# Kernel tuning notes

Measured on AMD Instinct MI355X. Metric: run time of the kernel, lower is better.

## Reference

```python
import math
import jax, jax.numpy as jnp
import numpy as np

EMBED = 1024
HEADS = 16
DEPTH = 12
HEAD_DIM = EMBED // HEADS // 2  # 32
LAMBDA_INIT = 0.8 - 0.6 * math.exp(-0.3 * DEPTH)


def setup_inputs() -> dict:
    key = jax.random.key(0)
    ks = jax.random.split(key, 11)
    B, T, S = 2, 2048, 2048
    std = 1.0 / math.sqrt(EMBED)
    return {
        "query_x": jax.random.normal(ks[0], (B, T, EMBED), jnp.float32),
        "kv_x": jax.random.normal(ks[1], (B, S, EMBED), jnp.float32),
        "Wq": jax.random.normal(ks[2], (EMBED, EMBED), jnp.float32) * std,
        "Wk": jax.random.normal(ks[3], (EMBED, EMBED), jnp.float32) * std,
        "Wv": jax.random.normal(ks[4], (EMBED, EMBED), jnp.float32) * std,
        "Wo": jax.random.normal(ks[5], (EMBED, EMBED), jnp.float32) * std,
        "lambda_q1": jax.random.normal(ks[6], (HEAD_DIM,), jnp.float32) * 0.1,
        "lambda_k1": jax.random.normal(ks[7], (HEAD_DIM,), jnp.float32) * 0.1,
        "lambda_q2": jax.random.normal(ks[8], (HEAD_DIM,), jnp.float32) * 0.1,
        "lambda_k2": jax.random.normal(ks[9], (HEAD_DIM,), jnp.float32) * 0.1,
        "subln_w": jnp.ones((2 * HEAD_DIM,), jnp.float32),
    }


def rms_norm(x, w, eps=1e-5):
    xf = x.astype(jnp.float32)
    out = xf * jax.lax.rsqrt(jnp.mean(xf * xf, axis=-1, keepdims=True) + eps)
    return out.astype(x.dtype) * w


def reference(query_x, kv_x, Wq, Wk, Wv, Wo, lambda_q1, lambda_k1, lambda_q2, lambda_k2, subln_w):
    B, T, _ = query_x.shape
    S = kv_x.shape[1]
    H, D = HEADS, HEAD_DIM
    scaling = D ** -0.5

    q = (query_x @ Wq).reshape(B, T, 2 * H, D).transpose(0, 2, 1, 3)  # [B,2H,T,D]
    k = (kv_x @ Wk).reshape(B, S, 2 * H, D).transpose(0, 2, 1, 3)     # [B,2H,S,D]
    v = (kv_x @ Wv).reshape(B, S, H, 2 * D).transpose(0, 2, 1, 3)     # [B,H,S,2D]

    scores = jnp.einsum("bhtd,bhsd->bhts", q * scaling, k)            # [B,2H,T,S]
    attn_w = jax.nn.softmax(scores.astype(jnp.float32), axis=-1).astype(scores.dtype)

    lambda_1 = jnp.exp(jnp.sum(lambda_q1 * lambda_k1).astype(jnp.float32))
    lambda_2 = jnp.exp(jnp.sum(lambda_q2 * lambda_k2).astype(jnp.float32))
    lambda_full = (lambda_1 - lambda_2 + LAMBDA_INIT).astype(q.dtype)

    attn_w = attn_w.reshape(B, H, 2, T, S)
    attn_w = attn_w[:, :, 0] - lambda_full * attn_w[:, :, 1]          # [B,H,T,S]

    attn = jnp.einsum("bhts,bhse->bhte", attn_w, v)                   # [B,H,T,2D]
    attn = rms_norm(attn, subln_w) * (1.0 - LAMBDA_INIT)
    attn = attn.transpose(0, 2, 1, 3).reshape(B, T, H * 2 * D)
    return attn @ Wo
```

## Files before the change

### kernel.cpp

```cpp
#include <hip/hip_runtime.h>
#include <stdint.h>


#define LAMBDA_INIT_F 0.7836057665316245f
#define OUT_SCALE_F   0.2163942334683755f
#define QK_SCALE_F    0.17677669529663687f
#define LOG2E_F       1.4426950408889634f

typedef _Float16 f16x8 __attribute__((ext_vector_type(8)));
typedef _Float16 f16x4 __attribute__((ext_vector_type(4)));
typedef _Float16 f16x2 __attribute__((ext_vector_type(2)));
typedef __fp16   h16x2 __attribute__((ext_vector_type(2)));
typedef float    f32x4 __attribute__((ext_vector_type(4)));
typedef float    f32x16 __attribute__((ext_vector_type(16)));

__device__ inline void gl_lds16(const void* g, void* l) {
  __builtin_amdgcn_global_load_lds(
      (const __attribute__((address_space(1))) void*)g,
      (__attribute__((address_space(3))) void*)l, 16, 0, 0);
}

__device__ inline f16x2 cvtpk(float a, float b) {
  h16x2 r = __builtin_amdgcn_cvt_pkrtz(a, b);
  return __builtin_bit_cast(f16x2, r);
}

__global__ __launch_bounds__(256) void prep(
    const float* __restrict__ qx, const float* __restrict__ kvx,
    const float* __restrict__ Wq, const float* __restrict__ Wk,
    const float* __restrict__ Wv, const float* __restrict__ Wo,
    const float* __restrict__ lq1, const float* __restrict__ lk1,
    const float* __restrict__ lq2, const float* __restrict__ lk2,
    _Float16* __restrict__ xq, _Float16* __restrict__ xkv,
    _Float16* __restrict__ WqT, _Float16* __restrict__ WkT,
    _Float16* __restrict__ WvT, _Float16* __restrict__ WoT,
    float* __restrict__ lamv) {
  __shared__ _Float16 t[64][65];
  const int bb = blockIdx.x;
  const int tid = threadIdx.x;
  if (bb < 8192) {
    const float* src = (bb < 4096) ? qx : kvx;
    _Float16* dst = (bb < 4096) ? xq : xkv;
    int i = ((bb & 4095) * 256 + tid) * 4;
    float4 v = *(const float4*)(src + i);
    f16x4 o;
    o[0] = (_Float16)v.x; o[1] = (_Float16)v.y;
    o[2] = (_Float16)v.z; o[3] = (_Float16)v.w;
    *(f16x4*)(dst + i) = o;
  } else if (bb < 9216) {
    const int idx = bb - 8192;
    const int w = idx >> 8, loc = idx & 255;
    const float* W = (w == 0) ? Wq : (w == 1) ? Wk : (w == 2) ? Wv : Wo;
    _Float16* Wt   = (w == 0) ? WqT : (w == 1) ? WkT : (w == 2) ? WvT : WoT;
    const float scale = (w == 0) ? QK_SCALE_F * LOG2E_F : 1.0f;
    const int nb = (loc & 15) * 64, kb2 = (loc >> 4) * 64;
#pragma unroll
    for (int p = 0; p < 16; ++p) {
      int i = p * 256 + tid;
      int r = i >> 6, c = i & 63;
      t[c][r] = (_Float16)(W[(size_t)(kb2 + r) * 1024 + nb + c] * scale);
    }
    __syncthreads();
#pragma unroll
    for (int p = 0; p < 16; ++p) {
      int i = p * 256 + tid;
      int r = i >> 6, c = i & 63;
      Wt[(size_t)(nb + r) * 1024 + kb2 + c] = t[r][c];
    }
  } else {
    if (tid < 64) {
      int l = tid;
      float a = (l < 32) ? lq1[l] * lk1[l] : 0.f;
      float b = (l < 32) ? lq2[l] * lk2[l] : 0.f;
#pragma unroll
      for (int m = 1; m < 64; m <<= 1) {
        a += __shfl_xor(a, m, 64);
        b += __shfl_xor(b, m, 64);
      }
      if (l == 0) lamv[0] = expf(a) - expf(b) + LAMBDA_INIT_F;
    }
  }
}

__global__ __launch_bounds__(256, 4) void gemmseg(
    const _Float16* __restrict__ A0, const _Float16* __restrict__ B0, _Float16* __restrict__ C0,
    const _Float16* __restrict__ A1, const _Float16* __restrict__ B1, _Float16* __restrict__ C1,
    const _Float16* __restrict__ A2, const _Float16* __restrict__ B2, _Float16* __restrict__ C2,
    int nseg, float* __restrict__ Cf32) {
  __shared__ alignas(16) _Float16 As[2][4096];
  __shared__ alignas(16) _Float16 Bs[2][4096];
  const int tid = threadIdx.x;
  const int lane = tid & 63, wid = tid >> 6;
  const int g = lane >> 4, ln = lane & 15;
  const int wm = wid >> 1, wn = wid & 1;

  const int nwg = nseg << 8;
  const int b0 = blockIdx.x;
  const int swz = (b0 & 7) * (nwg >> 3) + (b0 >> 3);
  const int seg = swz >> 8, loc = swz & 255;
  const _Float16 *A, *B;
  _Float16* C;
  if (seg == 0)      { A = A0; B = B0; C = C0; }
  else if (seg == 1) { A = A1; B = B1; C = C1; }
  else               { A = A2; B = B2; C = C2; }
  int bm, bn, N;
  if (seg == 2) { N = 4096; bm = (loc >> 5) << 7; bn = (loc & 31) << 7; }
  else          { N = 1024; bm = (loc >> 3) << 7; bn = (loc & 7) << 7; }
  const int K = 1024;

  f32x4 acc[4][4];
#pragma unroll
  for (int i = 0; i < 4; ++i)
#pragma unroll
    for (int j = 0; j < 4; ++j) acc[i][j] = (f32x4){0.f, 0.f, 0.f, 0.f};

  int aoff[4], boff[4];
#pragma unroll
  for (int i = 0; i < 4; ++i) {
    int r = wm * 64 + i * 16 + ln;
    aoff[i] = r * 32 + (((g + ((r >> 1) & 3)) & 3) << 3);
    r = wn * 64 + i * 16 + ln;
    boff[i] = r * 32 + (((g + ((r >> 1) & 3)) & 3) << 3);
  }

  auto STAGE = [&](int buf, int kt) {
#pragma unroll
    for (int l2 = 0; l2 < 2; ++l2) {
      int ci = l2 * 256 + wid * 64 + lane;
      int r = ci >> 2, cp = ci & 3;
      int c = (cp - ((r >> 1) & 3)) & 3;
      gl_lds16(A + (size_t)(bm + r) * K + kt + c * 8,
               (void*)&As[buf][l2 * 2048 + wid * 512]);
      gl_lds16(B + (size_t)(bn + r) * K + kt + c * 8,
               (void*)&Bs[buf][l2 * 2048 + wid * 512]);
    }
  };

  STAGE(0, 0);
  __syncthreads();
  int buf = 0;
  for (int kt = 0; kt < K; kt += 32) {
    if (kt + 32 < K) STAGE(buf ^ 1, kt + 32);
    f16x8 af[4], bf[4];
#pragma unroll
    for (int i = 0; i < 4; ++i) {
      af[i] = *(const f16x8*)(&As[buf][aoff[i]]);
      bf[i] = *(const f16x8*)(&Bs[buf][boff[i]]);
    }
#pragma unroll
    for (int i = 0; i < 4; ++i)
#pragma unroll
      for (int j = 0; j < 4; ++j)
        acc[i][j] = __builtin_amdgcn_mfma_f32_16x16x32_f16(af[i], bf[j], acc[i][j], 0, 0, 0);
    __syncthreads();
    buf ^= 1;
  }

#pragma unroll
  for (int i = 0; i < 4; ++i) {
#pragma unroll
    for (int j = 0; j < 4; ++j) {
      int grow = bm + wm * 64 + i * 16 + g * 4;
      int gcol = bn + wn * 64 + j * 16 + ln;
#pragma unroll
      for (int r = 0; r < 4; ++r) {
        if (Cf32) Cf32[(size_t)(grow + r) * N + gcol] = acc[i][j][r];
        else      C[(size_t)(grow + r) * N + gcol] = (_Float16)acc[i][j][r];
      }
    }
  }
}

__global__ __launch_bounds__(512, 4) void diffattn(const _Float16* __restrict__ qb,
                                                   const _Float16* __restrict__ kb,
                                                   const _Float16* __restrict__ vT,
                                                   const float* __restrict__ lam_p,
                                                   const float* __restrict__ subw,
                                                   _Float16* __restrict__ attn16) {
  __shared__ alignas(16) _Float16 stg[2][8192];

  const int tid = threadIdx.x;
  const int lane = tid & 63, wid = tid >> 6;
  const int q32 = lane & 31;
  const int hl = lane >> 5;
  const int wq = wid & 1;
  const int comp = (wid >> 1) & 1;
  const int sh = wid >> 2;
  const int bid = blockIdx.x;
  const int wg = ((bid & 7) << 7) | (bid >> 3);
  const int qt = wg & 31;
  const int h = (wg >> 5) & 15;
  const int b = wg >> 9;
  const int trow = qt * 64 + wq * 32 + q32;

  const _Float16* qp = qb + ((size_t)b * 2048 + trow) * 1024 + (2 * h + comp) * 32 + hl * 8;
  f16x8 qf_0 = *(const f16x8*)(qp);
  f16x8 qf_1 = *(const f16x8*)(qp + 16);

  const _Float16* kg;
  {
    const int r = (wid & 1) * 16 + (lane >> 2);
    const int pos = lane & 3;
    const int c = (pos - ((r >> 1) & 3)) & 3;
    kg = kb + ((size_t)b * 2048 + (size_t)(wid >> 2) * 1024 + r) * 1024 +
         (2 * h + ((wid >> 1) & 1)) * 32 + c * 8;
  }
  const _Float16* vg;
  {
    const int e = wid * 8 + (lane >> 3);
    const int pos = lane & 7;
    const int ca = (pos - (e & 7)) & 7;
    vg = vT + ((size_t)(h * 64 + e)) * 4096 + (size_t)b * 2048 +
         (ca >> 2) * 1024 + (ca & 3) * 8;
  }

  const int kreg = (sh * 2 + comp) * 1024;
  const int sk = (q32 >> 1) & 3;
  const int ko0 = kreg + q32 * 32 + ((hl + sk) & 3) * 8;
  const int ko1 = kreg + q32 * 32 + ((2 + hl + sk) & 3) * 8;
  const int e7 = q32 & 7;
  const int vb0 = 4096 + q32 * 64 + hl * 4;
  const int vp0 = ((sh * 4 + 0 + e7) & 7) * 8;
  const int vp1 = ((sh * 4 + 1 + e7) & 7) * 8;
  const int vp2 = ((sh * 4 + 2 + e7) & 7) * 8;
  const int vp3 = ((sh * 4 + 3 + e7) & 7) * 8;

  f32x16 O[2] = {};
  float m = 0.f, l = 0.f;
  const f32x16 zf = {};

  auto STAGE = [&](int buf, int it) {
    gl_lds16(kg + (size_t)it * 32768, (void*)&stg[buf][wid * 512]);
    gl_lds16(vg + it * 32,            (void*)&stg[buf][4096 + wid * 512]);
  };

  auto PROC = [&](int buf) {
    const _Float16* sb = &stg[buf][0];
    f16x8 Kf0 = *(const f16x8*)(sb + ko0);
    f16x8 Kf1 = *(const f16x8*)(sb + ko1);

    __builtin_amdgcn_s_setprio(1);
    f32x16 st = __builtin_amdgcn_mfma_f32_32x32x16_f16(Kf0, qf_0, zf, 0, 0, 0);
    st = __builtin_amdgcn_mfma_f32_32x32x16_f16(Kf1, qf_1, st, 0, 0, 0);
    __builtin_amdgcn_s_setprio(0);

    float p[16];
#pragma unroll
    for (int i = 0; i < 16; ++i) p[i] = __builtin_amdgcn_exp2f(st[i]);
    float s8[8];
#pragma unroll
    for (int i = 0; i < 8; ++i) s8[i] = p[2 * i] + p[2 * i + 1];
#pragma unroll
    for (int i = 0; i < 4; ++i) s8[i] += s8[i + 4];
    float rs = (s8[0] + s8[1]) + (s8[2] + s8[3]);
    l += rs + __shfl_xor(rs, 32, 64);

    union { f16x8 v; f16x2 h2[4]; } pb0, pb1;
    pb0.h2[0] = cvtpk(p[0], p[1]);   pb0.h2[1] = cvtpk(p[2], p[3]);
    pb0.h2[2] = cvtpk(p[4], p[5]);   pb0.h2[3] = cvtpk(p[6], p[7]);
    pb1.h2[0] = cvtpk(p[8], p[9]);   pb1.h2[1] = cvtpk(p[10], p[11]);
    pb1.h2[2] = cvtpk(p[12], p[13]); pb1.h2[3] = cvtpk(p[14], p[15]);

    const _Float16* v0 = sb + vb0;
    const _Float16* v1 = sb + vb0 + 2048;
    union { f16x8 v; f16x4 h4[2]; } va00, va01, va10, va11;
    va00.h4[0] = *(const f16x4*)(v0 + vp0); va00.h4[1] = *(const f16x4*)(v0 + vp1);
    va01.h4[0] = *(const f16x4*)(v1 + vp0); va01.h4[1] = *(const f16x4*)(v1 + vp1);
    va10.h4[0] = *(const f16x4*)(v0 + vp2); va10.h4[1] = *(const f16x4*)(v0 + vp3);
    va11.h4[0] = *(const f16x4*)(v1 + vp2); va11.h4[1] = *(const f16x4*)(v1 + vp3);

    __builtin_amdgcn_s_setprio(1);
    O[0] = __builtin_amdgcn_mfma_f32_32x32x16_f16(va00.v, pb0.v, O[0], 0, 0, 0);
    O[1] = __builtin_amdgcn_mfma_f32_32x32x16_f16(va01.v, pb0.v, O[1], 0, 0, 0);
    O[0] = __builtin_amdgcn_mfma_f32_32x32x16_f16(va10.v, pb1.v, O[0], 0, 0, 0);
    O[1] = __builtin_amdgcn_mfma_f32_32x32x16_f16(va11.v, pb1.v, O[1], 0, 0, 0);
    __builtin_amdgcn_s_setprio(0);
  };

  STAGE(0, 0);
  __syncthreads();
  int buf = 0;
  for (int it = 0; it < 32; ++it) {
    if (it + 1 < 32) STAGE(buf ^ 1, it + 1);
    PROC(buf);
    __syncthreads();
    buf ^= 1;
  }

  float* pay = (float*)&stg[0][0];
  _Float16* o2s = (_Float16*)(pay + 2 * 64 * 34);

  if (comp == 1 && sh == 1) {
    float* d = pay + (wq * 64 + lane) * 34;
#pragma unroll
    for (int t2 = 0; t2 < 2; ++t2)
#pragma unroll
      for (int i = 0; i < 16; ++i) d[t2 * 16 + i] = O[t2][i];
    d[32] = m; d[33] = l;
  }
  __syncthreads();
  if (comp == 1 && sh == 0) {
    const float* d = pay + (wq * 64 + lane) * 34;
    float mb = d[32], lb = d[33];
    float mn = fmaxf(m, mb);
    float ca = __builtin_amdgcn_exp2f(m - mn);
    float cb = __builtin_amdgcn_exp2f(mb - mn);
    m = mn; l = l * ca + lb * cb;
#pragma unroll
    for (int t2 = 0; t2 < 2; ++t2)
#pragma unroll
      for (int i = 0; i < 16; ++i) O[t2][i] = O[t2][i] * ca + d[t2 * 16 + i] * cb;
  }
  __syncthreads();
  if (comp == 0 && sh == 1) {
    float* d = pay + (wq * 64 + lane) * 34;
#pragma unroll
    for (int t2 = 0; t2 < 2; ++t2)
#pragma unroll
      for (int i = 0; i < 16; ++i) d[t2 * 16 + i] = O[t2][i];
    d[32] = m; d[33] = l;
  }
  if (comp == 1 && sh == 0) {
    float rl = 1.f / l;
    _Float16* d = o2s + (wq * 64 + lane) * 32;
#pragma unroll
    for (int t2 = 0; t2 < 2; ++t2)
#pragma unroll
      for (int i = 0; i < 16; ++i) d[t2 * 16 + i] = (_Float16)(O[t2][i] * rl);
  }
  __syncthreads();
  if (comp != 0 || sh != 0) return;

  {
    const float* d = pay + (wq * 64 + lane) * 34;
    float mb = d[32], lb = d[33];
    float mn = fmaxf(m, mb);
    float ca = __builtin_amdgcn_exp2f(m - mn);
    float cb = __builtin_amdgcn_exp2f(mb - mn);
    l = l * ca + lb * cb;
#pragma unroll
    for (int t2 = 0; t2 < 2; ++t2)
#pragma unroll
      for (int i = 0; i < 16; ++i) O[t2][i] = O[t2][i] * ca + d[t2 * 16 + i] * cb;
  }

  const float lam = lam_p[0];
  const _Float16* d2 = o2s + (wq * 64 + lane) * 32;
  float rl = 1.f / l;
  float x[2][16];
  float ssq = 0.f;
#pragma unroll
  for (int et = 0; et < 2; ++et)
#pragma unroll
    for (int i = 0; i < 16; ++i) {
      float v = O[et][i] * rl - lam * (float)d2[et * 16 + i];
      x[et][i] = v;
      ssq += v * v;
    }
  ssq += __shfl_xor(ssq, 32, 64);
  float rms = rsqrtf(ssq * (1.f / 64.f) + 1e-5f) * OUT_SCALE_F;

  _Float16* orow = attn16 + ((size_t)b * 2048 + trow) * 1024 + h * 64;
#pragma unroll
  for (int et = 0; et < 2; ++et)
#pragma unroll
    for (int grp = 0; grp < 4; ++grp) {
      int e0 = et * 32 + grp * 8 + 4 * hl;
      float4 w = *(const float4*)(subw + e0);
      f16x4 o;
      o[0] = (_Float16)(x[et][grp * 4 + 0] * rms * w.x);
      o[1] = (_Float16)(x[et][grp * 4 + 1] * rms * w.y);
      o[2] = (_Float16)(x[et][grp * 4 + 2] * rms * w.z);
      o[3] = (_Float16)(x[et][grp * 4 + 3] * rms * w.w);
      *(f16x4*)(orow + e0) = o;
    }
}

extern "C" void kernel_launch(void* const* d_in, const int* in_sizes, int n_in,
                              void* d_out, int out_size, void* d_ws, size_t ws_size,
                              hipStream_t stream) {
  const float* query_x = (const float*)d_in[0];
  const float* kv_x    = (const float*)d_in[1];
  const float* Wq      = (const float*)d_in[2];
  const float* Wk      = (const float*)d_in[3];
  const float* Wv      = (const float*)d_in[4];
  const float* Wo      = (const float*)d_in[5];
  const float* lq1     = (const float*)d_in[6];
  const float* lk1     = (const float*)d_in[7];
  const float* lq2     = (const float*)d_in[8];
  const float* lk2     = (const float*)d_in[9];
  const float* subw    = (const float*)d_in[10];
  float* out = (float*)d_out;

  const size_t NX = (size_t)4096 * 1024;
  const size_t NW = (size_t)1024 * 1024;
  _Float16* xq  = (_Float16*)d_ws;
  _Float16* xkv = xq  + NX;
  _Float16* WqT = xkv + NX;
  _Float16* WkT = WqT + NW;
  _Float16* WvT = WkT + NW;
  _Float16* WoT = WvT + NW;
  _Float16* qb  = WoT + NW;
  _Float16* kbf = qb  + NX;
  _Float16* vTb = kbf + NX;
  _Float16* a16 = vTb + NX;
  float* lamv   = (float*)(a16 + NX);

  prep<<<9217, 256, 0, stream>>>(query_x, kv_x, Wq, Wk, Wv, Wo,
                                 lq1, lk1, lq2, lk2,
                                 xq, xkv, WqT, WkT, WvT, WoT, lamv);

  gemmseg<<<768, 256, 0, stream>>>(xq, WqT, qb,
                                   xkv, WkT, kbf,
                                   WvT, xkv, vTb,
                                   3, nullptr);

  diffattn<<<1024, 512, 0, stream>>>(qb, kbf, vTb, lamv, subw, a16);

  gemmseg<<<256, 256, 0, stream>>>(a16, WoT, nullptr,
                                   nullptr, nullptr, nullptr,
                                   nullptr, nullptr, nullptr,
                                   1, out);
}
```

Baseline: 156.0 us.

## Process two query sub-tiles per attention block to reuse staged K/V tiles

Each attention workgroup now covers 128 query rows instead of 64. Every wave holds two Q fragments and issues twice the MFMAs against each staged K/V tile, which halves the grid and the global-to-LDS K/V traffic per query row. The combine epilogue drops the unused running-max rescaling and becomes plain sums, then runs twice, once per sub-tile. In exchange the kernel needs more registers (launch bounds lowered to 2 blocks per SM) and has fewer blocks in flight, which may reduce latency hiding.

```diff
diff --git a/kernel.cpp b/kernel.cpp
--- a/kernel.cpp
+++ b/kernel.cpp
@@ -171,7 +171,7 @@
   }
 }
 
-__global__ __launch_bounds__(512, 4) void diffattn(const _Float16* __restrict__ qb,
+__global__ __launch_bounds__(512, 2) void diffattn(const _Float16* __restrict__ qb,
                                                    const _Float16* __restrict__ kb,
                                                    const _Float16* __restrict__ vT,
                                                    const float* __restrict__ lam_p,
@@ -187,15 +187,18 @@
   const int comp = (wid >> 1) & 1;
   const int sh = wid >> 2;
   const int bid = blockIdx.x;
-  const int wg = ((bid & 7) << 7) | (bid >> 3);
-  const int qt = wg & 31;
-  const int h = (wg >> 5) & 15;
-  const int b = wg >> 9;
-  const int trow = qt * 64 + wq * 32 + q32;
-
-  const _Float16* qp = qb + ((size_t)b * 2048 + trow) * 1024 + (2 * h + comp) * 32 + hl * 8;
-  f16x8 qf_0 = *(const f16x8*)(qp);
-  f16x8 qf_1 = *(const f16x8*)(qp + 16);
+  const int wg = ((bid & 7) << 6) | (bid >> 3);
+  const int qt = wg & 15;
+  const int h = (wg >> 4) & 15;
+  const int b = wg >> 8;
+  const int trowA = qt * 128 + wq * 64 + q32;
+
+  const _Float16* qpA = qb + ((size_t)b * 2048 + trowA) * 1024 + (2 * h + comp) * 32 + hl * 8;
+  f16x8 qfA0 = *(const f16x8*)(qpA);
+  f16x8 qfA1 = *(const f16x8*)(qpA + 16);
+  const _Float16* qpB = qpA + (size_t)32 * 1024;
+  f16x8 qfB0 = *(const f16x8*)(qpB);
+  f16x8 qfB1 = *(const f16x8*)(qpB + 16);
 
   const _Float16* kg;
   {
@@ -225,8 +228,8 @@
   const int vp2 = ((sh * 4 + 2 + e7) & 7) * 8;
   const int vp3 = ((sh * 4 + 3 + e7) & 7) * 8;
 
-  f32x16 O[2] = {};
-  float m = 0.f, l = 0.f;
+  f32x16 OA[2] = {}, OB[2] = {};
+  float lpA = 0.f, lpB = 0.f;
   const f32x16 zf = {};
 
   auto STAGE = [&](int buf, int it) {
@@ -240,40 +243,64 @@
     f16x8 Kf1 = *(const f16x8*)(sb + ko1);
 
     __builtin_amdgcn_s_setprio(1);
-    f32x16 st = __builtin_amdgcn_mfma_f32_32x32x16_f16(Kf0, qf_0, zf, 0, 0, 0);
-    st = __builtin_amdgcn_mfma_f32_32x32x16_f16(Kf1, qf_1, st, 0, 0, 0);
+    f32x16 stA = __builtin_amdgcn_mfma_f32_32x32x16_f16(Kf0, qfA0, zf, 0, 0, 0);
+    stA = __builtin_amdgcn_mfma_f32_32x32x16_f16(Kf1, qfA1, stA, 0, 0, 0);
+    f32x16 stB = __builtin_amdgcn_mfma_f32_32x32x16_f16(Kf0, qfB0, zf, 0, 0, 0);
+    stB = __builtin_amdgcn_mfma_f32_32x32x16_f16(Kf1, qfB1, stB, 0, 0, 0);
     __builtin_amdgcn_s_setprio(0);
 
-    float p[16];
-#pragma unroll
-    for (int i = 0; i < 16; ++i) p[i] = __builtin_amdgcn_exp2f(st[i]);
-    float s8[8];
-#pragma unroll
-    for (int i = 0; i < 8; ++i) s8[i] = p[2 * i] + p[2 * i + 1];
-#pragma unroll
-    for (int i = 0; i < 4; ++i) s8[i] += s8[i + 4];
-    float rs = (s8[0] + s8[1]) + (s8[2] + s8[3]);
-    l += rs + __shfl_xor(rs, 32, 64);
-
-    union { f16x8 v; f16x2 h2[4]; } pb0, pb1;
-    pb0.h2[0] = cvtpk(p[0], p[1]);   pb0.h2[1] = cvtpk(p[2], p[3]);
-    pb0.h2[2] = cvtpk(p[4], p[5]);   pb0.h2[3] = cvtpk(p[6], p[7]);
-    pb1.h2[0] = cvtpk(p[8], p[9]);   pb1.h2[1] = cvtpk(p[10], p[11]);
-    pb1.h2[2] = cvtpk(p[12], p[13]); pb1.h2[3] = cvtpk(p[14], p[15]);
+    float pA[16], pB[16];
+#pragma unroll
+    for (int i = 0; i < 16; ++i) pA[i] = __builtin_amdgcn_exp2f(stA[i]);
+#pragma unroll
+    for (int i = 0; i < 16; ++i) pB[i] = __builtin_amdgcn_exp2f(stB[i]);
+    {
+      float s8[8];
+#pragma unroll
+      for (int i = 0; i < 8; ++i) s8[i] = pA[2 * i] + pA[2 * i + 1];
+#pragma unroll
+      for (int i = 0; i < 4; ++i) s8[i] += s8[i + 4];
+      lpA += (s8[0] + s8[1]) + (s8[2] + s8[3]);
+    }
+    {
+      float s8[8];
+#pragma unroll
+      for (int i = 0; i < 8; ++i) s8[i] = pB[2 * i] + pB[2 * i + 1];
+#pragma unroll
+      for (int i = 0; i < 4; ++i) s8[i] += s8[i + 4];
+      lpB += (s8[0] + s8[1]) + (s8[2] + s8[3]);
+    }
+
+    union { f16x8 v; f16x2 h2[4]; } pbA0, pbA1, pbB0, pbB1;
+    pbA0.h2[0] = cvtpk(pA[0], pA[1]);   pbA0.h2[1] = cvtpk(pA[2], pA[3]);
+    pbA0.h2[2] = cvtpk(pA[4], pA[5]);   pbA0.h2[3] = cvtpk(pA[6], pA[7]);
+    pbA1.h2[0] = cvtpk(pA[8], pA[9]);   pbA1.h2[1] = cvtpk(pA[10], pA[11]);
+    pbA1.h2[2] = cvtpk(pA[12], pA[13]); pbA1.h2[3] = cvtpk(pA[14], pA[15]);
+    pbB0.h2[0] = cvtpk(pB[0], pB[1]);   pbB0.h2[1] = cvtpk(pB[2], pB[3]);
+    pbB0.h2[2] = cvtpk(pB[4], pB[5]);   pbB0.h2[3] = cvtpk(pB[6], pB[7]);
+    pbB1.h2[0] = cvtpk(pB[8], pB[9]);   pbB1.h2[1] = cvtpk(pB[10], pB[11]);
+    pbB1.h2[2] = cvtpk(pB[12], pB[13]); pbB1.h2[3] = cvtpk(pB[14], pB[15]);
 
     const _Float16* v0 = sb + vb0;
     const _Float16* v1 = sb + vb0 + 2048;
-    union { f16x8 v; f16x4 h4[2]; } va00, va01, va10, va11;
-    va00.h4[0] = *(const f16x4*)(v0 + vp0); va00.h4[1] = *(const f16x4*)(v0 + vp1);
-    va01.h4[0] = *(const f16x4*)(v1 + vp0); va01.h4[1] = *(const f16x4*)(v1 + vp1);
-    va10.h4[0] = *(const f16x4*)(v0 + vp2); va10.h4[1] = *(const f16x4*)(v0 + vp3);
-    va11.h4[0] = *(const f16x4*)(v1 + vp2); va11.h4[1] = *(const f16x4*)(v1 + vp3);
-
+    union { f16x8 v; f16x4 h4[2]; } va0, va1;
+
+    va0.h4[0] = *(const f16x4*)(v0 + vp0); va0.h4[1] = *(const f16x4*)(v0 + vp1);
+    va1.h4[0] = *(const f16x4*)(v1 + vp0); va1.h4[1] = *(const f16x4*)(v1 + vp1);
     __builtin_amdgcn_s_setprio(1);
-    O[0] = __builtin_amdgcn_mfma_f32_32x32x16_f16(va00.v, pb0.v, O[0], 0, 0, 0);
-    O[1] = __builtin_amdgcn_mfma_f32_32x32x16_f16(va01.v, pb0.v, O[1], 0, 0, 0);
-    O[0] = __builtin_amdgcn_mfma_f32_32x32x16_f16(va10.v, pb1.v, O[0], 0, 0, 0);
-    O[1] = __builtin_amdgcn_mfma_f32_32x32x16_f16(va11.v, pb1.v, O[1], 0, 0, 0);
+    OA[0] = __builtin_amdgcn_mfma_f32_32x32x16_f16(va0.v, pbA0.v, OA[0], 0, 0, 0);
+    OA[1] = __builtin_amdgcn_mfma_f32_32x32x16_f16(va1.v, pbA0.v, OA[1], 0, 0, 0);
+    OB[0] = __builtin_amdgcn_mfma_f32_32x32x16_f16(va0.v, pbB0.v, OB[0], 0, 0, 0);
+    OB[1] = __builtin_amdgcn_mfma_f32_32x32x16_f16(va1.v, pbB0.v, OB[1], 0, 0, 0);
+    __builtin_amdgcn_s_setprio(0);
+
+    va0.h4[0] = *(const f16x4*)(v0 + vp2); va0.h4[1] = *(const f16x4*)(v0 + vp3);
+    va1.h4[0] = *(const f16x4*)(v1 + vp2); va1.h4[1] = *(const f16x4*)(v1 + vp3);
+    __builtin_amdgcn_s_setprio(1);
+    OA[0] = __builtin_amdgcn_mfma_f32_32x32x16_f16(va0.v, pbA1.v, OA[0], 0, 0, 0);
+    OA[1] = __builtin_amdgcn_mfma_f32_32x32x16_f16(va1.v, pbA1.v, OA[1], 0, 0, 0);
+    OB[0] = __builtin_amdgcn_mfma_f32_32x32x16_f16(va0.v, pbB1.v, OB[0], 0, 0, 0);
+    OB[1] = __builtin_amdgcn_mfma_f32_32x32x16_f16(va1.v, pbB1.v, OB[1], 0, 0, 0);
     __builtin_amdgcn_s_setprio(0);
   };
 
@@ -287,29 +314,29 @@
     buf ^= 1;
   }
 
+  float lA = lpA + __shfl_xor(lpA, 32, 64);
+  float lB = lpB + __shfl_xor(lpB, 32, 64);
+
   float* pay = (float*)&stg[0][0];
   _Float16* o2s = (_Float16*)(pay + 2 * 64 * 34);
+  const float lam = lam_p[0];
 
   if (comp == 1 && sh == 1) {
     float* d = pay + (wq * 64 + lane) * 34;
 #pragma unroll
     for (int t2 = 0; t2 < 2; ++t2)
 #pragma unroll
-      for (int i = 0; i < 16; ++i) d[t2 * 16 + i] = O[t2][i];
-    d[32] = m; d[33] = l;
+      for (int i = 0; i < 16; ++i) d[t2 * 16 + i] = OA[t2][i];
+    d[32] = lA;
   }
   __syncthreads();
   if (comp == 1 && sh == 0) {
     const float* d = pay + (wq * 64 + lane) * 34;
-    float mb = d[32], lb = d[33];
-    float mn = fmaxf(m, mb);
-    float ca = __builtin_amdgcn_exp2f(m - mn);
-    float cb = __builtin_amdgcn_exp2f(mb - mn);
-    m = mn; l = l * ca + lb * cb;
-#pragma unroll
-    for (int t2 = 0; t2 < 2; ++t2)
-#pragma unroll
-      for (int i = 0; i < 16; ++i) O[t2][i] = O[t2][i] * ca + d[t2 * 16 + i] * cb;
+    lA += d[32];
+#pragma unroll
+    for (int t2 = 0; t2 < 2; ++t2)
+#pragma unroll
+      for (int i = 0; i < 16; ++i) OA[t2][i] += d[t2 * 16 + i];
   }
   __syncthreads();
   if (comp == 0 && sh == 1) {
@@ -317,63 +344,131 @@
 #pragma unroll
     for (int t2 = 0; t2 < 2; ++t2)
 #pragma unroll
-      for (int i = 0; i < 16; ++i) d[t2 * 16 + i] = O[t2][i];
-    d[32] = m; d[33] = l;
+      for (int i = 0; i < 16; ++i) d[t2 * 16 + i] = OA[t2][i];
+    d[32] = lA;
   }
   if (comp == 1 && sh == 0) {
-    float rl = 1.f / l;
+    float rl = 1.f / lA;
     _Float16* d = o2s + (wq * 64 + lane) * 32;
 #pragma unroll
     for (int t2 = 0; t2 < 2; ++t2)
 #pragma unroll
-      for (int i = 0; i < 16; ++i) d[t2 * 16 + i] = (_Float16)(O[t2][i] * rl);
-  }
-  __syncthreads();
-  if (comp != 0 || sh != 0) return;
-
-  {
+      for (int i = 0; i < 16; ++i) d[t2 * 16 + i] = (_Float16)(OA[t2][i] * rl);
+  }
+  __syncthreads();
+  if (comp == 0 && sh == 0) {
     const float* d = pay + (wq * 64 + lane) * 34;
-    float mb = d[32], lb = d[33];
-    float mn = fmaxf(m, mb);
-    float ca = __builtin_amdgcn_exp2f(m - mn);
-    float cb = __builtin_amdgcn_exp2f(mb - mn);
-    l = l * ca + lb * cb;
-#pragma unroll
-    for (int t2 = 0; t2 < 2; ++t2)
-#pragma unroll
-      for (int i = 0; i < 16; ++i) O[t2][i] = O[t2][i] * ca + d[t2 * 16 + i] * cb;
-  }
-
-  const float lam = lam_p[0];
-  const _Float16* d2 = o2s + (wq * 64 + lane) * 32;
-  float rl = 1.f / l;
-  float x[2][16];
-  float ssq = 0.f;
-#pragma unroll
-  for (int et = 0; et < 2; ++et)
-#pragma unroll
-    for (int i = 0; i < 16; ++i) {
-      float v = O[et][i] * rl - lam * (float)d2[et * 16 + i];
-      x[et][i] = v;
-      ssq += v * v;
-    }
-  ssq += __shfl_xor(ssq, 32, 64);
-  float rms = rsqrtf(ssq * (1.f / 64.f) + 1e-5f) * OUT_SCALE_F;
-
-  _Float16* orow = attn16 + ((size_t)b * 2048 + trow) * 1024 + h * 64;
-#pragma unroll
-  for (int et = 0; et < 2; ++et)
-#pragma unroll
-    for (int grp = 0; grp < 4; ++grp) {
-      int e0 = et * 32 + grp * 8 + 4 * hl;
-      float4 w = *(const float4*)(subw + e0);
-      f16x4 o;
-      o[0] = (_Float16)(x[et][grp * 4 + 0] * rms * w.x);
-      o[1] = (_Float16)(x[et][grp * 4 + 1] * rms * w.y);
-      o[2] = (_Float16)(x[et][grp * 4 + 2] * rms * w.z);
-      o[3] = (_Float16)(x[et][grp * 4 + 3] * rms * w.w);
-      *(f16x4*)(orow + e0) = o;
-    }
+    lA += d[32];
+#pragma unroll
+    for (int t2 = 0; t2 < 2; ++t2)
+#pragma unroll
+      for (int i = 0; i < 16; ++i) OA[t2][i] += d[t2 * 16 + i];
+
+    const _Float16* d2 = o2s + (wq * 64 + lane) * 32;
+    float rl = 1.f / lA;
+    float x[2][16];
+    float ssq = 0.f;
+#pragma unroll
+    for (int et = 0; et < 2; ++et)
+#pragma unroll
+      for (int i = 0; i < 16; ++i) {
+        float v = OA[et][i] * rl - lam * (float)d2[et * 16 + i];
+        x[et][i] = v;
+        ssq += v * v;
+      }
+    ssq += __shfl_xor(ssq, 32, 64);
+    float rms = rsqrtf(ssq * (1.f / 64.f) + 1e-5f) * OUT_SCALE_F;
+
+    _Float16* orow = attn16 + ((size_t)b * 2048 + trowA) * 1024 + h * 64;
+#pragma unroll
+    for (int et = 0; et < 2; ++et)
+#pragma unroll
+      for (int grp = 0; grp < 4; ++grp) {
+        int e0 = et * 32 + grp * 8 + 4 * hl;
+        float4 w = *(const float4*)(subw + e0);
+        f16x4 o;
+        o[0] = (_Float16)(x[et][grp * 4 + 0] * rms * w.x);
+        o[1] = (_Float16)(x[et][grp * 4 + 1] * rms * w.y);
+        o[2] = (_Float16)(x[et][grp * 4 + 2] * rms * w.z);
+        o[3] = (_Float16)(x[et][grp * 4 + 3] * rms * w.w);
+        *(f16x4*)(orow + e0) = o;
+      }
+  }
+  __syncthreads();
+
+  if (comp == 1 && sh == 1) {
+    float* d = pay + (wq * 64 + lane) * 34;
+#pragma unroll
+    for (int t2 = 0; t2 < 2; ++t2)
+#pragma unroll
+      for (int i = 0; i < 16; ++i) d[t2 * 16 + i] = OB[t2][i];
+    d[32] = lB;
+  }
+  __syncthreads();
+  if (comp == 1 && sh == 0) {
+    const float* d = pay + (wq * 64 + lane) * 34;
+    lB += d[32];
+#pragma unroll
+    for (int t2 = 0; t2 < 2; ++t2)
+#pragma unroll
+      for (int i = 0; i < 16; ++i) OB[t2][i] += d[t2 * 16 + i];
+  }
+  __syncthreads();
+  if (comp == 0 && sh == 1) {
+    float* d = pay + (wq * 64 + lane) * 34;
+#pragma unroll
+    for (int t2 = 0; t2 < 2; ++t2)
+#pragma unroll
+      for (int i = 0; i < 16; ++i) d[t2 * 16 + i] = OB[t2][i];
+    d[32] = lB;
+  }
+  if (comp == 1 && sh == 0) {
+    float rl = 1.f / lB;
+    _Float16* d = o2s + (wq * 64 + lane) * 32;
+#pragma unroll
+    for (int t2 = 0; t2 < 2; ++t2)
+#pragma unroll
+      for (int i = 0; i < 16; ++i) d[t2 * 16 + i] = (_Float16)(OB[t2][i] * rl);
+  }
+  __syncthreads();
+  if (comp == 0 && sh == 0) {
+    const float* d = pay + (wq * 64 + lane) * 34;
+    lB += d[32];
+#pragma unroll
+    for (int t2 = 0; t2 < 2; ++t2)
+#pragma unroll
+      for (int i = 0; i < 16; ++i) OB[t2][i] += d[t2 * 16 + i];
+
+    const _Float16* d2 = o2s + (wq * 64 + lane) * 32;
+    float rl = 1.f / lB;
+    float x[2][16];
+    float ssq = 0.f;
+#pragma unroll
+    for (int et = 0; et < 2; ++et)
+#pragma unroll
+      for (int i = 0; i < 16; ++i) {
+        float v = OB[et][i] * rl - lam * (float)d2[et * 16 + i];
+        x[et][i] = v;
+        ssq += v * v;
+      }
+    ssq += __shfl_xor(ssq, 32, 64);
+    float rms = rsqrtf(ssq * (1.f / 64.f) + 1e-5f) * OUT_SCALE_F;
+
+    _Float16* orow = attn16 + ((size_t)b * 2048 + trowA + 32) * 1024 + h * 64;
+#pragma unroll
+    for (int et = 0; et < 2; ++et)
+#pragma unroll
+      for (int grp = 0; grp < 4; ++grp) {
+        int e0 = et * 32 + grp * 8 + 4 * hl;
+        float4 w = *(const float4*)(subw + e0);
+        f16x4 o;
+        o[0] = (_Float16)(x[et][grp * 4 + 0] * rms * w.x);
+        o[1] = (_Float16)(x[et][grp * 4 + 1] * rms * w.y);
+        o[2] = (_Float16)(x[et][grp * 4 + 2] * rms * w.z);
+        o[3] = (_Float16)(x[et][grp * 4 + 3] * rms * w.w);
+        *(f16x4*)(orow + e0) = o;
+      }
+  }
 }
 
 extern "C" void kernel_launch(void* const* d_in, const int* in_sizes, int n_in,
@@ -415,7 +510,7 @@
                                    WvT, xkv, vTb,
                                    3, nullptr);
 
-  diffattn<<<1024, 512, 0, stream>>>(qb, kbf, vTb, lamv, subw, a16);
+  diffattn<<<512, 512, 0, stream>>>(qb, kbf, vTb, lamv, subw, a16);
 
   gemmseg<<<256, 256, 0, stream>>>(a16, WoT, nullptr,
                                    nullptr, nullptr, nullptr,
```

Result: faster. 147.7 us (-5.3%).
